# Performance work log

Measured on AMD Instinct MI355X. Metric: run time of the kernel, lower is better.

## Reference

```python
import jax, jax.numpy as jnp
import numpy as np

B, T, C, H, TT = 8, 1024, 512, 8, 4  # batch, seq, n_embd, n_head, total_timestep
D = C // H


def setup_inputs() -> dict:
    key = jax.random.key(0)
    ks = jax.random.split(key, 4)
    s = 1.0 / np.sqrt(C)
    return {
        "x": jax.random.normal(ks[0], (B, T, C), jnp.float32),
        "padding_mask": jax.random.bernoulli(ks[1], 0.1, (TT, T)),  # bool
        "W_qkv": jax.random.normal(ks[2], (C, 3 * C), jnp.float32) * s,
        "b_qkv": jnp.zeros((3 * C,), jnp.float32),
        "W_proj": jax.random.normal(ks[3], (C, C), jnp.float32) * s,
        "b_proj": jnp.zeros((C,), jnp.float32),
    }


def reference(x, padding_mask, W_qkv, b_qkv, W_proj, b_proj):
    # fused QKV projection
    qkv = x @ W_qkv + b_qkv                       # [B,T,3C]
    q, k, v = jnp.split(qkv, 3, axis=-1)
    q = q.reshape(B, T, H, D)
    k = k.reshape(B, T, H, D)
    v = v.reshape(B, T, H, D)

    # mask: causal OR padding (True = attend), replicating torch semantics
    causal = jnp.tril(jnp.ones((T, T), bool))                 # [T,T]
    m = causal[None] | padding_mask[:, :, None]               # [TT,T,T]
    mask = jnp.broadcast_to(m[None], (B // TT, TT, T, T)).reshape(B, 1, T, T)

    scores = jnp.einsum("bqhd,bkhd->bhqk", q, k) * (1.0 / np.sqrt(D))
    scores = jnp.where(mask, scores, jnp.float32(-1e30))
    attn = jax.nn.softmax(scores, axis=-1)                    # [B,H,T,T]
    y = jnp.einsum("bhqk,bkhd->bqhd", attn, v).reshape(B, T, C)
    return y @ W_proj + b_proj
```

## Files before the change

### kernel.cpp

```cpp
#include <hip/hip_runtime.h>
#include <hip/hip_bf16.h>

#define BB 8
#define TT_ 4
#define TSEQ 1024
#define CEMB 512
#define NH 8
#define HD 64

typedef __attribute__((ext_vector_type(8))) short bf16x8;
typedef __attribute__((ext_vector_type(4))) float f32x4;
typedef __attribute__((ext_vector_type(16))) float f32x16;

#define AS1 __attribute__((address_space(1)))
#define AS3 __attribute__((address_space(3)))

__device__ __forceinline__ void gload_lds16(const void* g, void* l) {
  __builtin_amdgcn_global_load_lds((const AS1 unsigned int*)g, (AS3 unsigned int*)l, 16, 0, 0);
}

__device__ __forceinline__ short f2b(float f) {
  union { float f; unsigned u; } v; v.f = f;
  unsigned r = v.u + 0x7FFFu + ((v.u >> 16) & 1u);
  return (short)(r >> 16);
}

__device__ __forceinline__ unsigned pack2(float a, float b) {
  unsigned r;
  asm("v_cvt_pk_bf16_f32 %0, %1, %2" : "=v"(r) : "v"(a), "v"(b));
  return r;
}

__global__ __launch_bounds__(256) void k_mask(const void* __restrict__ pin, int* __restrict__ pme,
                                              int* __restrict__ perm, int* __restrict__ chunk_nkt) {
  __shared__ int bad_f32, any_f32, bad_i32, any_i32, bad_u16, any_u16;
  if (threadIdx.x == 0) { bad_f32 = any_f32 = bad_i32 = any_i32 = bad_u16 = any_u16 = 0; }
  __syncthreads();
  const unsigned char* pb = (const unsigned char*)pin;
  const float* pf = (const float*)pin;
  const int* pi = (const int*)pin;
  const unsigned short* ph = (const unsigned short*)pin;
  for (int i = threadIdx.x; i < 1024; i += 256) {
    float fv = pf[i];
    if (fv != 0.0f && fv != 1.0f) bad_f32 = 1;
    if (fv == 1.0f) any_f32 = 1;
    int iv = pi[i];
    if (iv != 0 && iv != 1) bad_i32 = 1;
    if (iv == 1) any_i32 = 1;
  }
  for (int i = threadIdx.x; i < 2048; i += 256) {
    unsigned short hv = ph[i];
    if (hv != 0 && hv != 0x3F80u && hv != 0x3C00u) bad_u16 = 1;
    if (hv == 0x3F80u || hv == 0x3C00u) any_u16 = 1;
  }
  __syncthreads();
  int mode = 3;
  if (!bad_f32 && any_f32) mode = 0;
  else if (!bad_i32 && any_i32) mode = 1;
  else if (!bad_u16 && any_u16) mode = 2;
  for (int i = threadIdx.x; i < TT_ * TSEQ; i += 256) {
    int v;
    if (mode == 0)      v = (pf[i] != 0.0f);
    else if (mode == 1) v = (pi[i] != 0);
    else if (mode == 2) v = (ph[i] != 0);
    else                v = (pb[i] != 0);
    pme[i] = v;
  }
  __syncthreads();

  const int w = threadIdx.x >> 6, lane = threadIdx.x & 63;
  {
    const int* rowp = pme + w * 1024;
    unsigned long long bal[16];
    int npm = 0;
#pragma unroll
    for (int g = 0; g < 16; ++g) {
      bal[g] = __ballot(rowp[g * 64 + lane] != 0);
      npm += __popcll(bal[g]);
    }
    int off_non = 0, off_pm = 1024 - npm;
#pragma unroll
    for (int g = 0; g < 16; ++g) {
      unsigned long long m = bal[g];
      int below = __popcll(m & ((1ull << lane) - 1ull));
      int ispm = (int)((m >> lane) & 1ull);
      int pos = ispm ? (off_pm + below) : (off_non + lane - below);
      perm[w * 1024 + pos] = g * 64 + lane;
      int c = __popcll(m);
      off_pm += c; off_non += 64 - c;
    }
  }
  __syncthreads();
  {
    const int tt = w, c = (lane >> 3) & 7, seg = lane & 7;
    int mx = 0;
#pragma unroll
    for (int i = 0; i < 16; ++i) {
      int q = perm[tt * 1024 + c * 128 + seg * 16 + i];
      int need = pme[tt * 1024 + q] ? 16 : ((q >> 6) + 1);
      mx = mx > need ? mx : need;
    }
#pragma unroll
    for (int s = 1; s < 8; s <<= 1) {
      int o = __shfl_xor(mx, s, 64);
      mx = mx > o ? mx : o;
    }
    if (seg == 0) chunk_nkt[tt * 8 + c] = mx;
  }
}

__global__ __launch_bounds__(256) void k_cvt_x(const float* __restrict__ x, short* __restrict__ xb, int n4) {
  int i = blockIdx.x * 256 + threadIdx.x;
  if (i < n4) {
    float4 v = ((const float4*)x)[i];
    short4 o;
    o.x = f2b(v.x); o.y = f2b(v.y); o.z = f2b(v.z); o.w = f2b(v.w);
    ((short4*)xb)[i] = o;
  }
}

__global__ __launch_bounds__(256) void k_transpose2(const float* __restrict__ w0, short* __restrict__ t0,
                                                    const float* __restrict__ w1, short* __restrict__ t1) {
  const int z = blockIdx.z;
  if (z == 1 && blockIdx.x >= 8) return;
  const float* w = z ? w1 : w0;
  short* wt = z ? t1 : t0;
  const int N = z ? 512 : 1536, K = 512;
  __shared__ float t[64][65];
  const int tx = threadIdx.x & 15, ty = threadIdx.x >> 4;
  const int n0 = blockIdx.x * 64, k0 = blockIdx.y * 64;
#pragma unroll
  for (int i = 0; i < 4; ++i) {
    int kr = i * 16 + ty;
    float4 v = *(const float4*)&w[(size_t)(k0 + kr) * N + n0 + tx * 4];
    t[tx * 4 + 0][kr] = v.x; t[tx * 4 + 1][kr] = v.y;
    t[tx * 4 + 2][kr] = v.z; t[tx * 4 + 3][kr] = v.w;
  }
  __syncthreads();
#pragma unroll
  for (int i = 0; i < 4; ++i) {
    int nr = i * 16 + ty;
    short4 o;
    o.x = f2b(t[nr][tx * 4 + 0]); o.y = f2b(t[nr][tx * 4 + 1]);
    o.z = f2b(t[nr][tx * 4 + 2]); o.w = f2b(t[nr][tx * 4 + 3]);
    *(short4*)&wt[(size_t)(n0 + nr) * K + k0 + tx * 4] = o;
  }
}

template<int MODE, int NT>
__global__ __launch_bounds__(256) void k_gemm(
    const short* __restrict__ A, const short* __restrict__ Bt,
    const float* __restrict__ bias,
    short* __restrict__ qb, short* __restrict__ kb, short* __restrict__ vtb,
    float* __restrict__ fout)
{
  __shared__ short As[2][128 * 32];
  __shared__ short Bs[2][128 * 32];
  const int tid = threadIdx.x, lane = tid & 63, w = tid >> 6;
  const int wm = w >> 1, wn = w & 1;
  const int idp = (blockIdx.x & 7) * ((NT * 64) >> 3) + (blockIdx.x >> 3);
  const int n0 = (idp % NT) * 128, m0 = (idp / NT) * 128;
  f32x4 acc[4][4] = {};
  const char* Abase = (const char*)A + (size_t)m0 * 1024;
  const char* Bbase = (const char*)Bt + (size_t)n0 * 1024;
  const int rowL = w * 16 + (lane >> 2);
  const int colB = (lane & 3) * 16;

  auto stage = [&](int buf, int k0) {
#pragma unroll
    for (int is = 0; is < 2; ++is) {
      int row = is * 64 + rowL;
      gload_lds16(Abase + (size_t)row * 1024 + (size_t)(k0 * 2 + colB),
                  (char*)As[buf] + is * 4096 + w * 1024);
      gload_lds16(Bbase + (size_t)row * 1024 + (size_t)(k0 * 2 + colB),
                  (char*)Bs[buf] + is * 4096 + w * 1024);
    }
  };

  stage(0, 0);
  __syncthreads();
  int buf = 0;
  for (int k0 = 0; k0 < 512; k0 += 32) {
    if (k0 + 32 < 512) stage(buf ^ 1, k0 + 32);
    bf16x8 a[4], bfr[4];
#pragma unroll
    for (int mf = 0; mf < 4; ++mf)
      a[mf] = *(const bf16x8*)&As[buf][(wm * 64 + mf * 16 + (lane & 15)) * 32 + (lane >> 4) * 8];
#pragma unroll
    for (int nf = 0; nf < 4; ++nf)
      bfr[nf] = *(const bf16x8*)&Bs[buf][(wn * 64 + nf * 16 + (lane & 15)) * 32 + (lane >> 4) * 8];
#pragma unroll
    for (int mf = 0; mf < 4; ++mf)
#pragma unroll
      for (int nf = 0; nf < 4; ++nf)
        acc[mf][nf] = __builtin_amdgcn_mfma_f32_16x16x32_bf16(a[mf], bfr[nf], acc[mf][nf], 0, 0, 0);
    __syncthreads();
    buf ^= 1;
  }

#pragma unroll
  for (int nf = 0; nf < 4; ++nf) {
    const int n_g = n0 + wn * 64 + nf * 16 + (lane & 15);
    const float bv = bias[n_g];
    if (MODE == 0) {
      const int which = n_g >> 9;
      const int c = n_g & 511;
      const int h = c >> 6, d = c & 63;
      const float qsc = (which == 0) ? 0.18033688011112043f : 1.0f;
#pragma unroll
      for (int mf = 0; mf < 4; ++mf) {
        const int mb = m0 + wm * 64 + mf * 16 + ((lane >> 4) << 2);
        const int b = mb >> 10, t0 = mb & 1023;
        const int b8h = b * NH + h;
        if (which == 2) {
          short4 pk;
          pk.x = f2b(acc[mf][nf][0] + bv);
          pk.y = f2b(acc[mf][nf][1] + bv);
          pk.z = f2b(acc[mf][nf][2] + bv);
          pk.w = f2b(acc[mf][nf][3] + bv);
          *(short4*)&vtb[((size_t)b8h * HD + d) * TSEQ + t0] = pk;
        } else {
          short* dst = (which == 0) ? qb : kb;
          size_t base = ((size_t)b8h * TSEQ + t0) * HD + d;
#pragma unroll
          for (int r = 0; r < 4; ++r)
            dst[base + (size_t)r * HD] = f2b((acc[mf][nf][r] + bv) * qsc);
        }
      }
    } else {
#pragma unroll
      for (int mf = 0; mf < 4; ++mf) {
        const int mb = m0 + wm * 64 + mf * 16 + ((lane >> 4) << 2);
#pragma unroll
        for (int r = 0; r < 4; ++r)
          fout[(size_t)(mb + r) * 512 + n_g] = acc[mf][nf][r] + bv;
      }
    }
  }
}

__device__ __forceinline__ void pv_step(
    f32x16 p, int sub, int hi, int lq, const char* Vsb, f32x16& o0, f32x16& o1)
{
  unsigned P2[8];
#pragma unroll
  for (int i = 0; i < 8; ++i) P2[i] = pack2(p[2 * i], p[2 * i + 1]);
  unsigned e0 = __shfl_xor(hi ? P2[0] : P2[2], 32, 64);
  unsigned e1 = __shfl_xor(hi ? P2[1] : P2[3], 32, 64);
  unsigned e2 = __shfl_xor(hi ? P2[4] : P2[6], 32, 64);
  unsigned e3 = __shfl_xor(hi ? P2[5] : P2[7], 32, 64);
  union { unsigned u[4]; bf16x8 v; } f0, f1;
  f0.u[0] = hi ? e0 : P2[0]; f0.u[1] = hi ? e1 : P2[1];
  f0.u[2] = hi ? P2[2] : e0; f0.u[3] = hi ? P2[3] : e1;
  f1.u[0] = hi ? e2 : P2[4]; f1.u[1] = hi ? e3 : P2[5];
  f1.u[2] = hi ? P2[6] : e2; f1.u[3] = hi ? P2[7] : e3;
  __builtin_amdgcn_s_setprio(1);
#pragma unroll
  for (int dt = 0; dt < 2; ++dt) {
    int row = dt * 32 + lq;
    bf16x8 v0 = *(const bf16x8*)(Vsb + row * 128 + ((4 * sub + hi) ^ (row & 7)) * 16);
    bf16x8 v1 = *(const bf16x8*)(Vsb + row * 128 + ((4 * sub + 2 + hi) ^ (row & 7)) * 16);
    f32x16& o = dt ? o1 : o0;
    o = __builtin_amdgcn_mfma_f32_32x32x16_bf16(v0, f0.v, o, 0, 0, 0);
    o = __builtin_amdgcn_mfma_f32_32x32x16_bf16(v1, f1.v, o, 0, 0, 0);
  }
  __builtin_amdgcn_s_setprio(0);
}

__global__ __launch_bounds__(512) void k_attn(
    const short* __restrict__ qg, const short* __restrict__ kg,
    const short* __restrict__ vtg, const int* __restrict__ pme,
    const int* __restrict__ perm, const int* __restrict__ chunk_nkt,
    short* __restrict__ yb)
{
  __shared__ short Ks[3 * 64 * 64];
  __shared__ short Vs[3 * 64 * 64];
  const int tid = threadIdx.x, lane = tid & 63, w = tid >> 6;
  const int hi = lane >> 5, lq = lane & 31;
  const int id = blockIdx.x;
  const int bh = id & 63, b = bh >> 3, h = bh & 7, tt = b & 3;
  const int p = id >> 6;
  const int chunk = (w < 4) ? (7 - p) : p;
  const char* Qb = (const char*)(qg + (size_t)bh * TSEQ * HD);
  const char* Kb = (const char*)(kg + (size_t)bh * TSEQ * HD);
  const char* Vb = (const char*)(vtg + (size_t)bh * HD * TSEQ);

  const int stg_row = (w << 3) + (lane >> 3);
  const int stg_cl = (lane & 7) ^ ((lane >> 3) & 7);

  auto stage = [&](int buf, int kt) {
    gload_lds16(Kb + (size_t)(kt * 64 + stg_row) * 128 + stg_cl * 16,
                (char*)Ks + buf * 8192 + w * 1024);
    gload_lds16(Vb + (size_t)stg_row * 2048 + kt * 128 + stg_cl * 16,
                (char*)Vs + buf * 8192 + w * 1024);
  };

  stage(0, 0);
  stage(1, 1);

  const int nkt = chunk_nkt[tt * 8 + (7 - p)];
  const int q_g = perm[tt * 1024 + chunk * 128 + (w & 3) * 32 + lq];
  const int pmrow = pme[tt * TSEQ + q_g];

  int wmq = q_g, wnq = q_g;
#pragma unroll
  for (int s = 1; s < 32; s <<= 1) {
    wmq = max(wmq, __shfl_xor(wmq, s, 64));
    wnq = min(wnq, __shfl_xor(wnq, s, 64));
  }
  wmq = max(wmq, __shfl_xor(wmq, 32, 64));
  wnq = min(wnq, __shfl_xor(wnq, 32, 64));
  const int whaspm = __any(pmrow != 0);

  bf16x8 qf[4];
#pragma unroll
  for (int dk = 0; dk < 4; ++dk)
    qf[dk] = *(const bf16x8*)(Qb + (size_t)q_g * 128 + dk * 32 + hi * 16);

  float mrun = -__builtin_inff(), lrun = 0.0f;
  f32x16 o0 = {}, o1 = {};

  for (int kt = 0; kt < nkt; ++kt) {
    asm volatile("s_waitcnt vmcnt(2)\n\ts_barrier" ::: "memory");
    if (kt + 2 < nkt) stage((kt + 2) % 3, kt + 2);

    const int kb_ = kt * 64;
    if (kb_ <= wmq || whaspm) {
      const char* Ksb = (const char*)Ks + (kt % 3) * 8192;
      const char* Vsb = (const char*)Vs + (kt % 3) * 8192;

      f32x16 s0 = {}, s1 = {};
      __builtin_amdgcn_s_setprio(1);
#pragma unroll
      for (int dk = 0; dk < 4; ++dk) {
        int row0 = lq, row1 = 32 + lq;
        bf16x8 kf0 = *(const bf16x8*)(Ksb + row0 * 128 + ((2 * dk + hi) ^ (row0 & 7)) * 16);
        bf16x8 kf1 = *(const bf16x8*)(Ksb + row1 * 128 + ((2 * dk + hi) ^ (row1 & 7)) * 16);
        s0 = __builtin_amdgcn_mfma_f32_32x32x16_bf16(kf0, qf[dk], s0, 0, 0, 0);
        s1 = __builtin_amdgcn_mfma_f32_32x32x16_bf16(kf1, qf[dk], s1, 0, 0, 0);
      }
      __builtin_amdgcn_s_setprio(0);

      if (kb_ + 63 <= wnq) {
      } else if (kb_ > wmq) {
#pragma unroll
        for (int r = 0; r < 16; ++r) {
          s0[r] = pmrow ? s0[r] : -1e30f;
          s1[r] = pmrow ? s1[r] : -1e30f;
        }
      } else {
#pragma unroll
        for (int r = 0; r < 16; ++r) {
          int crow = (r & 3) + 8 * (r >> 2) + 4 * hi;
          s0[r] = ((kb_ + crow <= q_g) || pmrow) ? s0[r] : -1e30f;
          s1[r] = ((kb_ + 32 + crow <= q_g) || pmrow) ? s1[r] : -1e30f;
        }
      }

      float mx = s0[0];
#pragma unroll
      for (int r = 1; r < 16; ++r) mx = fmaxf(mx, s0[r]);
#pragma unroll
      for (int r = 0; r < 16; ++r) mx = fmaxf(mx, s1[r]);
      mx = fmaxf(mx, __shfl_xor(mx, 32, 64));
      if (!__all(mx <= mrun + 8.0f)) {
        float nm = fmaxf(mrun, mx);
        float sc = __builtin_amdgcn_exp2f(mrun - nm);
        lrun *= sc;
#pragma unroll
        for (int r = 0; r < 16; ++r) { o0[r] *= sc; o1[r] *= sc; }
        mrun = nm;
      }
      float rs = 0.0f;
#pragma unroll
      for (int r = 0; r < 16; ++r) { s0[r] = __builtin_amdgcn_exp2f(s0[r] - mrun); rs += s0[r]; }
#pragma unroll
      for (int r = 0; r < 16; ++r) { s1[r] = __builtin_amdgcn_exp2f(s1[r] - mrun); rs += s1[r]; }
      rs += __shfl_xor(rs, 32, 64);
      lrun += rs;

      pv_step(s0, 0, hi, lq, Vsb, o0, o1);
      pv_step(s1, 1, hi, lq, Vsb, o0, o1);
    }
  }

  const float inv = 1.0f / lrun;
  short* yrow = yb + ((size_t)b * TSEQ + q_g) * CEMB + h * HD;
#pragma unroll
  for (int dt = 0; dt < 2; ++dt) {
    const f32x16& o = dt ? o1 : o0;
#pragma unroll
    for (int g = 0; g < 4; ++g) {
      short4 pk;
      pk.x = f2b(o[4 * g + 0] * inv);
      pk.y = f2b(o[4 * g + 1] * inv);
      pk.z = f2b(o[4 * g + 2] * inv);
      pk.w = f2b(o[4 * g + 3] * inv);
      *(short4*)(yrow + dt * 32 + 8 * g + 4 * hi) = pk;
    }
  }
}

extern "C" void kernel_launch(void* const* d_in, const int* in_sizes, int n_in,
                              void* d_out, int out_size, void* d_ws, size_t ws_size,
                              hipStream_t stream) {
  const float* x     = (const float*)d_in[0];
  const void*  pmask = d_in[1];
  const float* Wqkv  = (const float*)d_in[2];
  const float* bqkv  = (const float*)d_in[3];
  const float* Wproj = (const float*)d_in[4];
  const float* bproj = (const float*)d_in[5];
  float* out = (float*)d_out;
  char* ws = (char*)d_ws;

  const size_t OFF_XB   = 0;
  const size_t OFF_WQT  = 8388608;
  const size_t OFF_WPT  = 9961472;
  const size_t OFF_Q    = 10485760;
  const size_t OFF_K    = 18874368;
  const size_t OFF_VT   = 27262976;
  const size_t OFF_Y    = 35651584;
  const size_t OFF_PM   = 44040192;
  const size_t OFF_PERM = 44056576;
  const size_t OFF_CNKT = 44072960;
  const size_t NEED     = 44073984;
  if (ws_size < NEED) return;

  short* xb  = (short*)(ws + OFF_XB);
  short* wqT = (short*)(ws + OFF_WQT);
  short* wpT = (short*)(ws + OFF_WPT);
  short* qb  = (short*)(ws + OFF_Q);
  short* kb  = (short*)(ws + OFF_K);
  short* vtb = (short*)(ws + OFF_VT);
  short* yb  = (short*)(ws + OFF_Y);
  int*   pme = (int*)(ws + OFF_PM);
  int*   prm = (int*)(ws + OFF_PERM);
  int*   cnk = (int*)(ws + OFF_CNKT);

  k_mask<<<dim3(1), dim3(256), 0, stream>>>(pmask, pme, prm, cnk);
  k_cvt_x<<<dim3(4096), dim3(256), 0, stream>>>(x, xb, (BB * TSEQ * CEMB) / 4);
  k_transpose2<<<dim3(24, 8, 2), dim3(256), 0, stream>>>(Wqkv, wqT, Wproj, wpT);
  k_gemm<0, 12><<<dim3(768), dim3(256), 0, stream>>>(xb, wqT, bqkv, qb, kb, vtb, nullptr);
  k_attn<<<dim3(256), dim3(512), 0, stream>>>(qb, kb, vtb, pme, prm, cnk, yb);
  k_gemm<1, 4><<<dim3(256), dim3(256), 0, stream>>>(yb, wpT, bproj, nullptr, nullptr, nullptr, out);
}
```

Baseline: 91.17 us.

## Triple-buffer GEMM with one barrier per step; split attention into 256-thread blocks

The GEMM kernel moves from double to triple LDS buffering. Each k-step now uses a single waitcnt plus barrier and issues the stage two steps ahead, and MFMA issue runs at raised priority. The attention kernel is split from 256 blocks of 8 waves, each pairing a long and a short causal chunk, into 512 blocks of 4 waves that each own one query chunk, with each block staging full K/V tiles itself. The aim is fewer barriers in the GEMM and more blocks for attention scheduling. The cost is more LDS per GEMM block and duplicated K/V staging loads across attention blocks, and the work pairing that balanced causal chunks is lost.

```diff
diff --git a/kernel.cpp b/kernel.cpp
--- a/kernel.cpp
+++ b/kernel.cpp
@@ -154,8 +154,8 @@
     short* __restrict__ qb, short* __restrict__ kb, short* __restrict__ vtb,
     float* __restrict__ fout)
 {
-  __shared__ short As[2][128 * 32];
-  __shared__ short Bs[2][128 * 32];
+  __shared__ short As[3][128 * 32];
+  __shared__ short Bs[3][128 * 32];
   const int tid = threadIdx.x, lane = tid & 63, w = tid >> 6;
   const int wm = w >> 1, wn = w & 1;
   const int idp = (blockIdx.x & 7) * ((NT * 64) >> 3) + (blockIdx.x >> 3);
@@ -166,36 +166,39 @@
   const int rowL = w * 16 + (lane >> 2);
   const int colB = (lane & 3) * 16;
 
-  auto stage = [&](int buf, int k0) {
+  auto stage = [&](int buf, int t) {
 #pragma unroll
     for (int is = 0; is < 2; ++is) {
       int row = is * 64 + rowL;
-      gload_lds16(Abase + (size_t)row * 1024 + (size_t)(k0 * 2 + colB),
+      gload_lds16(Abase + (size_t)row * 1024 + (size_t)(t * 64 + colB),
                   (char*)As[buf] + is * 4096 + w * 1024);
-      gload_lds16(Bbase + (size_t)row * 1024 + (size_t)(k0 * 2 + colB),
+      gload_lds16(Bbase + (size_t)row * 1024 + (size_t)(t * 64 + colB),
                   (char*)Bs[buf] + is * 4096 + w * 1024);
     }
   };
 
   stage(0, 0);
-  __syncthreads();
-  int buf = 0;
-  for (int k0 = 0; k0 < 512; k0 += 32) {
-    if (k0 + 32 < 512) stage(buf ^ 1, k0 + 32);
+  stage(1, 1);
+  for (int it = 0; it < 16; ++it) {
+    if (it < 15) asm volatile("s_waitcnt vmcnt(4)\n\ts_barrier" ::: "memory");
+    else         asm volatile("s_waitcnt vmcnt(0)\n\ts_barrier" ::: "memory");
+    if (it + 2 < 16) stage((it + 2) % 3, it + 2);
+    const short* Ab = As[it % 3];
+    const short* Bb = Bs[it % 3];
     bf16x8 a[4], bfr[4];
 #pragma unroll
     for (int mf = 0; mf < 4; ++mf)
-      a[mf] = *(const bf16x8*)&As[buf][(wm * 64 + mf * 16 + (lane & 15)) * 32 + (lane >> 4) * 8];
+      a[mf] = *(const bf16x8*)&Ab[(wm * 64 + mf * 16 + (lane & 15)) * 32 + (lane >> 4) * 8];
 #pragma unroll
     for (int nf = 0; nf < 4; ++nf)
-      bfr[nf] = *(const bf16x8*)&Bs[buf][(wn * 64 + nf * 16 + (lane & 15)) * 32 + (lane >> 4) * 8];
+      bfr[nf] = *(const bf16x8*)&Bb[(wn * 64 + nf * 16 + (lane & 15)) * 32 + (lane >> 4) * 8];
+    __builtin_amdgcn_s_setprio(1);
 #pragma unroll
     for (int mf = 0; mf < 4; ++mf)
 #pragma unroll
       for (int nf = 0; nf < 4; ++nf)
         acc[mf][nf] = __builtin_amdgcn_mfma_f32_16x16x32_bf16(a[mf], bfr[nf], acc[mf][nf], 0, 0, 0);
-    __syncthreads();
-    buf ^= 1;
+    __builtin_amdgcn_s_setprio(0);
   }
 
 #pragma unroll
@@ -267,20 +270,19 @@
   __builtin_amdgcn_s_setprio(0);
 }
 
-__global__ __launch_bounds__(512) void k_attn(
+__global__ __launch_bounds__(256) void k_attn(
     const short* __restrict__ qg, const short* __restrict__ kg,
     const short* __restrict__ vtg, const int* __restrict__ pme,
     const int* __restrict__ perm, const int* __restrict__ chunk_nkt,
     short* __restrict__ yb)
 {
-  __shared__ short Ks[3 * 64 * 64];
-  __shared__ short Vs[3 * 64 * 64];
+  __shared__ short Ks[3][64 * 64];
+  __shared__ short Vs[3][64 * 64];
   const int tid = threadIdx.x, lane = tid & 63, w = tid >> 6;
   const int hi = lane >> 5, lq = lane & 31;
   const int id = blockIdx.x;
   const int bh = id & 63, b = bh >> 3, h = bh & 7, tt = b & 3;
-  const int p = id >> 6;
-  const int chunk = (w < 4) ? (7 - p) : p;
+  const int chunk = 7 - (id >> 6);
   const char* Qb = (const char*)(qg + (size_t)bh * TSEQ * HD);
   const char* Kb = (const char*)(kg + (size_t)bh * TSEQ * HD);
   const char* Vb = (const char*)(vtg + (size_t)bh * HD * TSEQ);
@@ -289,27 +291,29 @@
   const int stg_cl = (lane & 7) ^ ((lane >> 3) & 7);
 
   auto stage = [&](int buf, int kt) {
-    gload_lds16(Kb + (size_t)(kt * 64 + stg_row) * 128 + stg_cl * 16,
-                (char*)Ks + buf * 8192 + w * 1024);
-    gload_lds16(Vb + (size_t)stg_row * 2048 + kt * 128 + stg_cl * 16,
-                (char*)Vs + buf * 8192 + w * 1024);
+#pragma unroll
+    for (int is = 0; is < 2; ++is) {
+      int row = is * 32 + stg_row;
+      gload_lds16(Kb + (size_t)(kt * 64 + row) * 128 + stg_cl * 16,
+                  (char*)Ks[buf] + is * 4096 + w * 1024);
+      gload_lds16(Vb + (size_t)row * 2048 + kt * 128 + stg_cl * 16,
+                  (char*)Vs[buf] + is * 4096 + w * 1024);
+    }
   };
 
   stage(0, 0);
   stage(1, 1);
 
-  const int nkt = chunk_nkt[tt * 8 + (7 - p)];
-  const int q_g = perm[tt * 1024 + chunk * 128 + (w & 3) * 32 + lq];
+  const int nkt = chunk_nkt[tt * 8 + chunk];
+  const int q_g = perm[tt * 1024 + chunk * 128 + w * 32 + lq];
   const int pmrow = pme[tt * TSEQ + q_g];
 
   int wmq = q_g, wnq = q_g;
 #pragma unroll
-  for (int s = 1; s < 32; s <<= 1) {
+  for (int s = 1; s < 64; s <<= 1) {
     wmq = max(wmq, __shfl_xor(wmq, s, 64));
     wnq = min(wnq, __shfl_xor(wnq, s, 64));
   }
-  wmq = max(wmq, __shfl_xor(wmq, 32, 64));
-  wnq = min(wnq, __shfl_xor(wnq, 32, 64));
   const int whaspm = __any(pmrow != 0);
 
   bf16x8 qf[4];
@@ -321,13 +325,14 @@
   f32x16 o0 = {}, o1 = {};
 
   for (int kt = 0; kt < nkt; ++kt) {
-    asm volatile("s_waitcnt vmcnt(2)\n\ts_barrier" ::: "memory");
+    if (kt + 1 < nkt) asm volatile("s_waitcnt vmcnt(4)\n\ts_barrier" ::: "memory");
+    else              asm volatile("s_waitcnt vmcnt(0)\n\ts_barrier" ::: "memory");
     if (kt + 2 < nkt) stage((kt + 2) % 3, kt + 2);
 
     const int kb_ = kt * 64;
     if (kb_ <= wmq || whaspm) {
-      const char* Ksb = (const char*)Ks + (kt % 3) * 8192;
-      const char* Vsb = (const char*)Vs + (kt % 3) * 8192;
+      const char* Ksb = (const char*)Ks[kt % 3];
+      const char* Vsb = (const char*)Vs[kt % 3];
 
       f32x16 s0 = {}, s1 = {};
       __builtin_amdgcn_s_setprio(1);
@@ -441,6 +446,6 @@
   k_cvt_x<<<dim3(4096), dim3(256), 0, stream>>>(x, xb, (BB * TSEQ * CEMB) / 4);
   k_transpose2<<<dim3(24, 8, 2), dim3(256), 0, stream>>>(Wqkv, wqT, Wproj, wpT);
   k_gemm<0, 12><<<dim3(768), dim3(256), 0, stream>>>(xb, wqT, bqkv, qb, kb, vtb, nullptr);
-  k_attn<<<dim3(256), dim3(512), 0, stream>>>(qb, kb, vtb, pme, prm, cnk, yb);
+  k_attn<<<dim3(512), dim3(256), 0, stream>>>(qb, kb, vtb, pme, prm, cnk, yb);
   k_gemm<1, 4><<<dim3(256), dim3(256), 0, stream>>>(yb, wpT, bproj, nullptr, nullptr, nullptr, out);
 }
```

New measurement: 94.16 us. 3.3% more time.

## Split attention KV loop across two wave groups with LDS merge of partial softmax

Applied to the files above, without the earlier changes.

Each block now handles a single query chunk, and its two groups of four waves take even and odd KV tiles, each with its own double buffer. The two partial (max, sum, output) states are merged through LDS at the end. The grid doubles to 512 blocks. This replaces the earlier scheme that paired a heavy and a light chunk in one block, and aims at more parallelism and shorter per-wave KV chains for the causally unbalanced work. In exchange it adds a merge step, a full vmcnt(0) wait every iteration, and 64KB of LDS per block, which limits occupancy.

```diff
diff --git a/kernel.cpp b/kernel.cpp
--- a/kernel.cpp
+++ b/kernel.cpp
@@ -273,43 +273,43 @@
     const int* __restrict__ perm, const int* __restrict__ chunk_nkt,
     short* __restrict__ yb)
 {
-  __shared__ short Ks[3 * 64 * 64];
-  __shared__ short Vs[3 * 64 * 64];
+  __shared__ char smem[65536];
   const int tid = threadIdx.x, lane = tid & 63, w = tid >> 6;
+  const int g = w >> 2;
   const int hi = lane >> 5, lq = lane & 31;
   const int id = blockIdx.x;
   const int bh = id & 63, b = bh >> 3, h = bh & 7, tt = b & 3;
-  const int p = id >> 6;
-  const int chunk = (w < 4) ? (7 - p) : p;
+  const int chunk = 7 - (id >> 6);
   const char* Qb = (const char*)(qg + (size_t)bh * TSEQ * HD);
   const char* Kb = (const char*)(kg + (size_t)bh * TSEQ * HD);
   const char* Vb = (const char*)(vtg + (size_t)bh * HD * TSEQ);
 
-  const int stg_row = (w << 3) + (lane >> 3);
+  const int stg_row = ((w & 3) << 3) + (lane >> 3);
   const int stg_cl = (lane & 7) ^ ((lane >> 3) & 7);
 
   auto stage = [&](int buf, int kt) {
-    gload_lds16(Kb + (size_t)(kt * 64 + stg_row) * 128 + stg_cl * 16,
-                (char*)Ks + buf * 8192 + w * 1024);
-    gload_lds16(Vb + (size_t)stg_row * 2048 + kt * 128 + stg_cl * 16,
-                (char*)Vs + buf * 8192 + w * 1024);
+#pragma unroll
+    for (int is = 0; is < 2; ++is) {
+      int row = is * 32 + stg_row;
+      gload_lds16(Kb + (size_t)(kt * 64 + row) * 128 + stg_cl * 16,
+                  smem + buf * 8192 + is * 4096 + (w & 3) * 1024);
+      gload_lds16(Vb + (size_t)row * 2048 + kt * 128 + stg_cl * 16,
+                  smem + 32768 + buf * 8192 + is * 4096 + (w & 3) * 1024);
+    }
   };
 
-  stage(0, 0);
-  stage(1, 1);
-
-  const int nkt = chunk_nkt[tt * 8 + (7 - p)];
+  const int nkt = chunk_nkt[tt * 8 + chunk];
   const int q_g = perm[tt * 1024 + chunk * 128 + (w & 3) * 32 + lq];
   const int pmrow = pme[tt * TSEQ + q_g];
 
+  if (g < nkt) stage(g * 2, g);
+
   int wmq = q_g, wnq = q_g;
 #pragma unroll
-  for (int s = 1; s < 32; s <<= 1) {
+  for (int s = 1; s < 64; s <<= 1) {
     wmq = max(wmq, __shfl_xor(wmq, s, 64));
     wnq = min(wnq, __shfl_xor(wnq, s, 64));
   }
-  wmq = max(wmq, __shfl_xor(wmq, 32, 64));
-  wnq = min(wnq, __shfl_xor(wnq, 32, 64));
   const int whaspm = __any(pmrow != 0);
 
   bf16x8 qf[4];
@@ -317,17 +317,20 @@
   for (int dk = 0; dk < 4; ++dk)
     qf[dk] = *(const bf16x8*)(Qb + (size_t)q_g * 128 + dk * 32 + hi * 16);
 
-  float mrun = -__builtin_inff(), lrun = 0.0f;
+  float mrun = -1e30f, lrun = 0.0f;
   f32x16 o0 = {}, o1 = {};
 
-  for (int kt = 0; kt < nkt; ++kt) {
-    asm volatile("s_waitcnt vmcnt(2)\n\ts_barrier" ::: "memory");
-    if (kt + 2 < nkt) stage((kt + 2) % 3, kt + 2);
+  const int niter = (nkt + 1) >> 1;
+  for (int i = 0; i < niter; ++i) {
+    asm volatile("s_waitcnt vmcnt(0)" ::: "memory");
+    __builtin_amdgcn_s_barrier();
+    const int kt = 2 * i + g;
+    if (kt + 2 < nkt) stage(g * 2 + ((i + 1) & 1), kt + 2);
 
     const int kb_ = kt * 64;
-    if (kb_ <= wmq || whaspm) {
-      const char* Ksb = (const char*)Ks + (kt % 3) * 8192;
-      const char* Vsb = (const char*)Vs + (kt % 3) * 8192;
+    if (kt < nkt && (kb_ <= wmq || whaspm)) {
+      const char* Ksb = smem + (g * 2 + (i & 1)) * 8192;
+      const char* Vsb = smem + 32768 + (g * 2 + (i & 1)) * 8192;
 
       f32x16 s0 = {}, s1 = {};
       __builtin_amdgcn_s_setprio(1);
@@ -384,19 +387,39 @@
     }
   }
 
-  const float inv = 1.0f / lrun;
-  short* yrow = yb + ((size_t)b * TSEQ + q_g) * CEMB + h * HD;
-#pragma unroll
-  for (int dt = 0; dt < 2; ++dt) {
-    const f32x16& o = dt ? o1 : o0;
-#pragma unroll
-    for (int g = 0; g < 4; ++g) {
-      short4 pk;
-      pk.x = f2b(o[4 * g + 0] * inv);
-      pk.y = f2b(o[4 * g + 1] * inv);
-      pk.z = f2b(o[4 * g + 2] * inv);
-      pk.w = f2b(o[4 * g + 3] * inv);
-      *(short4*)(yrow + dt * 32 + 8 * g + 4 * hi) = pk;
+  __syncthreads();
+  float* mg = (float*)smem;
+  const int idx = (w & 3) * 64 + lane;
+  if (g == 1) {
+    mg[idx * 34 + 0] = mrun;
+    mg[idx * 34 + 1] = lrun;
+#pragma unroll
+    for (int j = 0; j < 16; ++j) mg[idx * 34 + 2 + j] = o0[j];
+#pragma unroll
+    for (int j = 0; j < 16; ++j) mg[idx * 34 + 18 + j] = o1[j];
+  }
+  __syncthreads();
+  if (g == 0) {
+    const float mB = mg[idx * 34 + 0], lB = mg[idx * 34 + 1];
+    const float m = fmaxf(mrun, mB);
+    const float wa = __builtin_amdgcn_exp2f(mrun - m);
+    const float wb = __builtin_amdgcn_exp2f(mB - m);
+    const float linv = 1.0f / (lrun * wa + lB * wb);
+    const float fa = wa * linv, fb = wb * linv;
+    short* yrow = yb + ((size_t)b * TSEQ + q_g) * CEMB + h * HD;
+#pragma unroll
+    for (int dt = 0; dt < 2; ++dt) {
+      const f32x16& o = dt ? o1 : o0;
+      const int ob = dt ? 18 : 2;
+#pragma unroll
+      for (int gg = 0; gg < 4; ++gg) {
+        short4 pk;
+        pk.x = f2b(o[4 * gg + 0] * fa + mg[idx * 34 + ob + 4 * gg + 0] * fb);
+        pk.y = f2b(o[4 * gg + 1] * fa + mg[idx * 34 + ob + 4 * gg + 1] * fb);
+        pk.z = f2b(o[4 * gg + 2] * fa + mg[idx * 34 + ob + 4 * gg + 2] * fb);
+        pk.w = f2b(o[4 * gg + 3] * fa + mg[idx * 34 + ob + 4 * gg + 3] * fb);
+        *(short4*)(yrow + dt * 32 + 8 * gg + 4 * hi) = pk;
+      }
     }
   }
 }
@@ -441,6 +464,6 @@
   k_cvt_x<<<dim3(4096), dim3(256), 0, stream>>>(x, xb, (BB * TSEQ * CEMB) / 4);
   k_transpose2<<<dim3(24, 8, 2), dim3(256), 0, stream>>>(Wqkv, wqT, Wproj, wpT);
   k_gemm<0, 12><<<dim3(768), dim3(256), 0, stream>>>(xb, wqT, bqkv, qb, kb, vtb, nullptr);
-  k_attn<<<dim3(256), dim3(512), 0, stream>>>(qb, kb, vtb, pme, prm, cnk, yb);
+  k_attn<<<dim3(512), dim3(512), 0, stream>>>(qb, kb, vtb, pme, prm, cnk, yb);
   k_gemm<1, 4><<<dim3(256), dim3(256), 0, stream>>>(yb, wpT, bproj, nullptr, nullptr, nullptr, out);
 }
```

Measured after the change: 88.18 us. 1.03x faster.
